# Kernel tuning notes

Hardware: AMD Instinct MI355X
Metric: run time of the kernel (lower is better)

## Reference

```python
import jax, jax.numpy as jnp
import numpy as np
from jax import lax

EPS = 1e-5

def bn(x, g, b):
    # training-mode BatchNorm2d over (N, H, W)
    m = jnp.mean(x, axis=(0, 2, 3), keepdims=True)
    v = jnp.var(x, axis=(0, 2, 3), keepdims=True)
    return (x - m) * lax.rsqrt(v + EPS) * g[None, :, None, None] + b[None, :, None, None]

def conv1x1(x, W):
    # x: [b,c,h,w], W: [o,c]
    return jnp.einsum('bchw,oc->bohw', x, W)

def conv3x3(x, W):
    # W: [o,i,3,3]
    return lax.conv_general_dilated(x, W, (1, 1), 'SAME',
                                    dimension_numbers=('NCHW', 'OIHW', 'NCHW'))

def lga(x, Wqkv, Wproj, g, b):
    # LinearGlobalAttention: O(N) global attention
    bsz, c, h, w = x.shape
    qkv = conv1x1(x, Wqkv)                       # [b, 3c, h, w]
    q, k, v = jnp.split(qkv, 3, axis=1)
    q = q.reshape(bsz, c, h * w)                 # [b, c, N]
    k = jax.nn.softmax(k.reshape(bsz, c, h * w), axis=-1)
    v = v.reshape(bsz, c, h * w)
    ctx = jnp.einsum('bcn,bdn->bcd', k, v)       # [b, c, c]
    out = jnp.einsum('bcd,bcn->bdn', ctx, q)     # context^T @ q -> [b, c, N]
    out = out.reshape(bsz, c, h, w)
    return jax.nn.relu(bn(conv1x1(out, Wproj), g, b))


def setup_inputs() -> dict:
    key = jax.random.key(0)
    ks = jax.random.split(key, 12)
    B, Cin, Cout, H, W = 16, 128, 256, 64, 64
    wd = Cout // 4  # branch width = 64
    sc = 0.05
    inp = {
        'x': jax.random.normal(ks[0], (B, Cin, H, W), jnp.float32),
        'W_sc': jax.random.normal(ks[1], (Cout, Cin), jnp.float32) * sc,
        'g_sc': jnp.ones((Cout,), jnp.float32),
        'b_sc': jnp.zeros((Cout,), jnp.float32),
        'W1': jax.random.normal(ks[2], (Cout, Cin), jnp.float32) * sc,
        'g1': jnp.ones((Cout,), jnp.float32),
        'b1': jnp.zeros((Cout,), jnp.float32),
        'Wb0': jax.random.normal(ks[3], (wd, wd), jnp.float32) * sc,
        'gb0': jnp.ones((wd,), jnp.float32),
        'bb0': jnp.zeros((wd,), jnp.float32),
        'Wb1': jax.random.normal(ks[4], (wd, wd, 3, 3), jnp.float32) * sc,
        'gb1': jnp.ones((wd,), jnp.float32),
        'bb1': jnp.zeros((wd,), jnp.float32),
        'Wqkv2': jax.random.normal(ks[5], (3 * wd, wd), jnp.float32) * sc,
        'Wproj2': jax.random.normal(ks[6], (wd, wd), jnp.float32) * sc,
        'ga2': jnp.ones((wd,), jnp.float32),
        'ba2': jnp.zeros((wd,), jnp.float32),
        'Wqkv3': jax.random.normal(ks[7], (3 * wd, wd), jnp.float32) * sc,
        'Wproj3': jax.random.normal(ks[8], (wd, wd), jnp.float32) * sc,
        'ga3': jnp.ones((wd,), jnp.float32),
        'ba3': jnp.zeros((wd,), jnp.float32),
        'W2': jax.random.normal(ks[9], (Cout, Cout), jnp.float32) * sc,
        'g2': jnp.ones((Cout,), jnp.float32),
        'b2': jnp.zeros((Cout,), jnp.float32),
    }
    return inp


def reference(x, W_sc, g_sc, b_sc, W1, g1, b1,
              Wb0, gb0, bb0, Wb1, gb1, bb1,
              Wqkv2, Wproj2, ga2, ba2,
              Wqkv3, Wproj3, ga3, ba3,
              W2, g2, b2):
    residual = bn(conv1x1(x, W_sc), g_sc, b_sc)
    h = jax.nn.relu(bn(conv1x1(x, W1), g1, b1))      # [b, 256, H, W]
    s0, s1, s2, s3 = jnp.split(h, 4, axis=1)          # width = 64 each
    o0 = jax.nn.relu(bn(conv1x1(s0, Wb0), gb0, bb0))  # k=1 branch
    o1 = jax.nn.relu(bn(conv3x3(s1, Wb1), gb1, bb1))  # k=3 branch
    o2 = lga(s2, Wqkv2, Wproj2, ga2, ba2)             # k=5 -> attention
    o3 = lga(s3, Wqkv3, Wproj3, ga3, ba3)             # k=7 -> attention
    out = jnp.concatenate([o0, o1, o2, o3], axis=1)
    out = bn(conv1x1(out, W2), g2, b2) + residual
    return jax.nn.relu(out)
```

## Files before the change

kernel.cpp:

```cpp
#include <hip/hip_runtime.h>
#include <hip/hip_bf16.h>

using bf16 = __hip_bfloat16;
typedef __bf16 bf16v8 __attribute__((ext_vector_type(8)));
typedef float f32x4 __attribute__((ext_vector_type(4)));

#define HW 4096
#define ROWS 65536

#define AS1 const __attribute__((address_space(1))) void*
#define AS3 __attribute__((address_space(3))) void*

__global__ void r5_init(float* __restrict__ stats) {
    int i = blockIdx.x * 256 + threadIdx.x;
    stats[i] = 0.f;
}

__global__ void r4_cvt_x(const float* __restrict__ x, bf16* __restrict__ xT) {
    __shared__ bf16 tile[64 * 65];
    int b = blockIdx.z, c0 = blockIdx.y * 64, n0 = blockIdx.x * 64;
    int t = threadIdx.x;
    for (int i = 0; i < 16; i++) {
        int idx = i * 256 + t;
        int cc = idx >> 6, nn = idx & 63;
        tile[nn * 65 + cc] = __float2bfloat16(x[((size_t)(b * 128 + c0 + cc)) * HW + n0 + nn]);
    }
    __syncthreads();
    for (int i = 0; i < 16; i++) {
        int idx = i * 256 + t;
        int nn = idx >> 6, cc = idx & 63;
        xT[((size_t)(b * HW + n0 + nn)) * 128 + c0 + cc] = tile[nn * 65 + cc];
    }
}

__global__ void r4_cvt_w(const float* __restrict__ Wsc, const float* __restrict__ W1,
                         const float* __restrict__ Wb0,
                         const float* __restrict__ Wqkv2, const float* __restrict__ Wqkv3,
                         const float* __restrict__ W2, bf16* __restrict__ wbase) {
    int i = blockIdx.x * 256 + threadIdx.x;
    const float* s; int off;
    if      (i < 32768)  { s = Wsc;   off = i; }
    else if (i < 65536)  { s = W1;    off = i - 32768; }
    else if (i < 69632)  { s = Wb0;   off = i - 65536; }
    else if (i < 81920)  { s = Wqkv2; off = i - 69632; }
    else if (i < 94208)  { s = Wqkv3; off = i - 81920; }
    else                 { s = W2;    off = i - 94208; }
    wbase[i] = __float2bfloat16(s[off]);
}

__global__ void r4_pack3(const float* __restrict__ w, bf16* __restrict__ wp) {
    int i = blockIdx.x * 256 + threadIdx.x;
    int tap = i / 4096, rem = i % 4096;
    int o = rem >> 6, c = rem & 63;
    wp[i] = __float2bfloat16(w[(size_t)(o * 64 + c) * 9 + tap]);
}

__global__ __launch_bounds__(256) void r10_act(bf16* __restrict__ buf,
        const float* __restrict__ sums,
        const float* __restrict__ g0, const float* __restrict__ b0,
        const float* __restrict__ g1, const float* __restrict__ b1,
        const float* __restrict__ g2, const float* __restrict__ b2,
        const float* __restrict__ g3, const float* __restrict__ b3,
        int quarter) {
    __shared__ float scS[256], shS[256];
    int t = threadIdx.x;
    {
        const float *gp, *bp; int ci;
        if (quarter) {
            int qi = t >> 6; ci = t & 63;
            gp = qi == 0 ? g0 : qi == 1 ? g1 : qi == 2 ? g2 : g3;
            bp = qi == 0 ? b0 : qi == 1 ? b1 : qi == 2 ? b2 : b3;
        } else { gp = g0; bp = b0; ci = t; }
        float mean = sums[t] * (1.f / 65536.f);
        float var  = sums[256 + t] * (1.f / 65536.f) - mean * mean;
        float s = gp[ci] * rsqrtf(var + 1e-5f);
        scS[t] = s;
        shS[t] = bp[ci] - mean * s;
    }
    __syncthreads();
    long base = (long)blockIdx.x * 8192;
    int c0 = (t & 31) * 8;
#pragma unroll
    for (int i = 0; i < 4; i++) {
        long e = base + i * 2048 + t * 8;
        bf16v8 v = *(const bf16v8*)&buf[e];
#pragma unroll
        for (int j = 0; j < 8; j++) {
            float f = (float)v[j] * scS[c0 + j] + shS[c0 + j];
            v[j] = (__bf16)fmaxf(f, 0.f);
        }
        *(bf16v8*)&buf[e] = v;
    }
}

template <int KK>
__global__ __launch_bounds__(256) void ga_gemm(
        const bf16* __restrict__ A, int a_stride,
        const bf16* __restrict__ W, int w_stride,
        bf16* __restrict__ out0, bf16* __restrict__ out1, int split,
        int out_stride,
        float* __restrict__ stat0, float* __restrict__ stat1,
        int scol0, int scol1) {
    __shared__ bf16 shmem[128 * 136];
    __shared__ float sredS[256], sredQ[256];
    bf16* As = shmem;
    bf16* Ws = shmem + 8192;

    int t = threadIdx.x;
    int wave = t >> 6, lane = t & 63;
    int lo = lane & 15, quad = lane >> 4;
    int wr = wave >> 1, wc = wave & 1;
    int b = blockIdx.z;
    long grow = (long)b * HW + blockIdx.x * 128;
    int o0 = blockIdx.y * 128;
    const bf16* Wb = W + (long)o0 * w_stride;

    f32x4 acc[4][4];
#pragma unroll
    for (int m = 0; m < 4; m++)
#pragma unroll
        for (int n = 0; n < 4; n++) acc[m][n] = (f32x4){0.f, 0.f, 0.f, 0.f};

#pragma unroll
    for (int ph = 0; ph < KK / 64; ph++) {
        int k0 = ph * 64;
#pragma unroll
        for (int j = 0; j < 4; j++) {
            int i = j * 4 + wave;
            int ci = i * 64 + lane;
            int R = ci >> 3, cc = ci & 7;
            int sw = ((cc ^ (R & 7)) << 3);
            __builtin_amdgcn_global_load_lds(
                (AS1)(A + (grow + R) * (long)a_stride + k0 + sw),
                (AS3)(As + i * 512), 16, 0, 0);
            __builtin_amdgcn_global_load_lds(
                (AS1)(Wb + (long)R * w_stride + k0 + sw),
                (AS3)(Ws + i * 512), 16, 0, 0);
        }
        asm volatile("s_waitcnt vmcnt(0)" ::: "memory");
        __syncthreads();
#pragma unroll
        for (int ks = 0; ks < 64; ks += 32) {
            int kk = (ks >> 3) + quad;
            bf16v8 av[4], wv[4];
#pragma unroll
            for (int m = 0; m < 4; m++) {
                int R = wr * 64 + m * 16 + lo;
                av[m] = *(const bf16v8*)&As[R * 64 + ((kk ^ (R & 7)) << 3)];
            }
#pragma unroll
            for (int n = 0; n < 4; n++) {
                int R = wc * 64 + n * 16 + lo;
                wv[n] = *(const bf16v8*)&Ws[R * 64 + ((kk ^ (R & 7)) << 3)];
            }
#pragma unroll
            for (int m = 0; m < 4; m++)
#pragma unroll
                for (int n = 0; n < 4; n++)
                    acc[m][n] = __builtin_amdgcn_mfma_f32_16x16x32_bf16(av[m], wv[n], acc[m][n], 0, 0, 0);
        }
        __syncthreads();
    }

    bf16* Ot = shmem;
#pragma unroll
    for (int m = 0; m < 4; m++)
#pragma unroll
        for (int n = 0; n < 4; n++)
#pragma unroll
            for (int r = 0; r < 4; r++)
                Ot[(wr * 64 + m * 16 + quad * 4 + r) * 136 + wc * 64 + n * 16 + lo] =
                    __float2bfloat16(acc[m][n][r]);
    __syncthreads();
    bool low = o0 < split;
    bf16* op = low ? out0 : out1;
    int oc0 = low ? o0 : o0 - split;
#pragma unroll
    for (int i = 0; i < 8; i++) {
        int u = i * 256 + t;
        int lr = u >> 4, cg = u & 15;
        *(bf16v8*)&op[(grow + lr) * (long)out_stride + oc0 + cg * 8] =
            *(const bf16v8*)&Ot[lr * 136 + cg * 8];
    }
    if (stat0) {
        int c = t & 127, half = t >> 7;
        float s = 0.f, q = 0.f;
#pragma unroll
        for (int r = 0; r < 64; r++) {
            float v = __bfloat162float(Ot[(half * 64 + r) * 136 + c]);
            s += v; q += v * v;
        }
        sredS[t] = s; sredQ[t] = q;
        __syncthreads();
        if (t < 128) {
            float ss = sredS[t] + sredS[t + 128];
            float qq = sredQ[t] + sredQ[t + 128];
            float* st = low ? stat0 : stat1;
            int ci = (low ? scol0 + o0 : scol1 + o0 - split) + c;
            atomicAdd(&st[ci], ss);
            atomicAdd(&st[256 + ci], qq);
        }
    }
}

__global__ __launch_bounds__(256) void gb_gemm(
        const bf16* __restrict__ A, int a_stride,
        const bf16* __restrict__ W, long w_bstride,
        bf16* __restrict__ out, int out_stride,
        float* __restrict__ stat, int scol) {
    __shared__ bf16 shmem[256 * 64 + 64 * 64];
    __shared__ float sredS[256], sredQ[256];
    bf16* As = shmem;
    bf16* Ws = shmem + 256 * 64;

    int t = threadIdx.x;
    int wave = t >> 6, lane = t & 63;
    int lo = lane & 15, quad = lane >> 4;
    int b = blockIdx.z;
    long grow = (long)b * HW + blockIdx.x * 256;
    const bf16* Wb = W + (long)blockIdx.y * 4096 + (long)b * w_bstride;

    f32x4 acc[4][4];
#pragma unroll
    for (int m = 0; m < 4; m++)
#pragma unroll
        for (int n = 0; n < 4; n++) acc[m][n] = (f32x4){0.f, 0.f, 0.f, 0.f};

#pragma unroll
    for (int j = 0; j < 8; j++) {
        int ci = (j * 4 + wave) * 64 + lane;
        int R = ci >> 3, cc = ci & 7;
        __builtin_amdgcn_global_load_lds(
            (AS1)(A + (grow + R) * (long)a_stride + ((cc ^ (R & 7)) << 3)),
            (AS3)(As + (j * 4 + wave) * 512), 16, 0, 0);
    }
#pragma unroll
    for (int j = 0; j < 2; j++) {
        int ci = (j * 4 + wave) * 64 + lane;
        int R = ci >> 3, cc = ci & 7;
        __builtin_amdgcn_global_load_lds(
            (AS1)(Wb + R * 64 + ((cc ^ (R & 7)) << 3)),
            (AS3)(Ws + (j * 4 + wave) * 512), 16, 0, 0);
    }
    asm volatile("s_waitcnt vmcnt(0)" ::: "memory");
    __syncthreads();

#pragma unroll
    for (int ks = 0; ks < 64; ks += 32) {
        bf16v8 av[4], wv[4];
#pragma unroll
        for (int m = 0; m < 4; m++) {
            int R = wave * 64 + m * 16 + lo;
            av[m] = *(const bf16v8*)&As[R * 64 + ((((ks >> 3) + quad) ^ (R & 7)) << 3)];
        }
#pragma unroll
        for (int n = 0; n < 4; n++) {
            int o = n * 16 + lo;
            wv[n] = *(const bf16v8*)&Ws[o * 64 + ((((ks >> 3) + quad) ^ (o & 7)) << 3)];
        }
#pragma unroll
        for (int m = 0; m < 4; m++)
#pragma unroll
            for (int n = 0; n < 4; n++)
                acc[m][n] = __builtin_amdgcn_mfma_f32_16x16x32_bf16(av[m], wv[n], acc[m][n], 0, 0, 0);
    }
    __syncthreads();

    bf16* Ot = shmem;
#pragma unroll
    for (int m = 0; m < 4; m++)
#pragma unroll
        for (int n = 0; n < 4; n++)
#pragma unroll
            for (int r = 0; r < 4; r++)
                Ot[(wave * 64 + m * 16 + quad * 4 + r) * 72 + n * 16 + lo] =
                    __float2bfloat16(acc[m][n][r]);
    __syncthreads();
    int oc0 = blockIdx.y * 64;
#pragma unroll
    for (int i = 0; i < 8; i++) {
        int u = i * 256 + t;
        int lr = u >> 3, cg = u & 7;
        *(bf16v8*)&out[(grow + lr) * (long)out_stride + oc0 + cg * 8] =
            *(const bf16v8*)&Ot[lr * 72 + cg * 8];
    }
    if (stat) {
        int c = t & 63, qtr = t >> 6;
        float s = 0.f, q = 0.f;
#pragma unroll
        for (int r = 0; r < 64; r++) {
            float v = __bfloat162float(Ot[(qtr * 64 + r) * 72 + c]);
            s += v; q += v * v;
        }
        sredS[t] = s; sredQ[t] = q;
        __syncthreads();
        if (t < 64) {
            float ss = sredS[t] + sredS[t + 64] + sredS[t + 128] + sredS[t + 192];
            float qq = sredQ[t] + sredQ[t + 64] + sredQ[t + 128] + sredQ[t + 192];
            atomicAdd(&stat[scol + t], ss);
            atomicAdd(&stat[256 + scol + t], qq);
        }
    }
}

__global__ __launch_bounds__(256) void r12_conv3(
        const bf16* __restrict__ hT, const bf16* __restrict__ wp,
        bf16* __restrict__ obuf, float* __restrict__ stat) {
    __shared__ bf16 As[6 * 66 * 64];
    __shared__ bf16 Wt[9 * 64 * 64];
    __shared__ float sredS[256], sredQ[256];

    int t = threadIdx.x;
    int wave = t >> 6, lane = t & 63;
    int lo = lane & 15, quad = lane >> 4;
    int b = blockIdx.y, y0 = blockIdx.x * 4;

#pragma unroll
    for (int j = 0; j < 18; j++) {
        int i = j * 4 + wave;
        int ci = i * 64 + lane;
        int tap = ci >> 9, rem = ci & 511, o = rem >> 3, ck = rem & 7;
        __builtin_amdgcn_global_load_lds(
            (AS1)(wp + tap * 4096 + o * 64 + ((ck ^ (o & 7)) << 3)),
            (AS3)(Wt + i * 512), 16, 0, 0);
    }
#pragma unroll
    for (int j = 0; j < 12; j++) {
        int i = j * 4 + wave;
        int row = i >> 3, seg = i & 7;
        int yy = y0 - 1 + row;
        if (yy >= 0 && yy < 64) {
            int xg = seg * 8 + (lane >> 3), ck = lane & 7;
            __builtin_amdgcn_global_load_lds(
                (AS1)(hT + ((long)b * HW + yy * 64 + xg) * 256 + 64 + ((ck ^ (xg & 7)) << 3)),
                (AS3)(As + row * 4224 + 64 + seg * 512), 16, 0, 0);
        } else {
            *(bf16v8*)&As[row * 4224 + 64 + seg * 512 + lane * 8] = (bf16v8){0,0,0,0,0,0,0,0};
        }
    }
    if (t < 96) {
        int yr = t >> 4, side = (t >> 3) & 1, ck = t & 7;
        *(bf16v8*)&As[yr * 4224 + (side ? 65 : 0) * 64 + ck * 8] = (bf16v8){0,0,0,0,0,0,0,0};
    }
    asm volatile("s_waitcnt vmcnt(0)" ::: "memory");
    __syncthreads();

    f32x4 acc[4][4];
#pragma unroll
    for (int m = 0; m < 4; m++)
#pragma unroll
        for (int n = 0; n < 4; n++) acc[m][n] = (f32x4){0.f, 0.f, 0.f, 0.f};

#pragma unroll
    for (int tap = 0; tap < 9; tap++) {
        int dy = tap / 3 - 1, dx = tap % 3 - 1;
        int yr = wave + 1 + dy;
#pragma unroll
        for (int ks8 = 0; ks8 < 8; ks8 += 4) {
            int kk = ks8 + quad;
            bf16v8 wv[4];
#pragma unroll
            for (int ot = 0; ot < 4; ot++) {
                int o = ot * 16 + lo;
                wv[ot] = *(const bf16v8*)&Wt[tap * 4096 + o * 64 + ((kk ^ (o & 7)) << 3)];
            }
#pragma unroll
            for (int m = 0; m < 4; m++) {
                int xp = m * 16 + lo + dx;
                bf16v8 av = *(const bf16v8*)&As[yr * 4224 + (xp + 1) * 64 + ((kk ^ (xp & 7)) << 3)];
#pragma unroll
                for (int ot = 0; ot < 4; ot++)
                    acc[m][ot] = __builtin_amdgcn_mfma_f32_16x16x32_bf16(av, wv[ot], acc[m][ot], 0, 0, 0);
            }
        }
    }
    __syncthreads();

    bf16* Ot = As;
#pragma unroll
    for (int m = 0; m < 4; m++)
#pragma unroll
        for (int ot = 0; ot < 4; ot++)
#pragma unroll
            for (int r = 0; r < 4; r++)
                Ot[(wave * 64 + m * 16 + quad * 4 + r) * 72 + ot * 16 + lo] =
                    __float2bfloat16(acc[m][ot][r]);
    __syncthreads();

    long grow = (long)b * HW + y0 * 64;
#pragma unroll
    for (int i = 0; i < 8; i++) {
        int u = i * 256 + t;
        int lr = u >> 3, cg = u & 7;
        *(bf16v8*)&obuf[(grow + lr) * 256 + 64 + cg * 8] = *(const bf16v8*)&Ot[lr * 72 + cg * 8];
    }
    {
        int c = t & 63, qtr = t >> 6;
        float s = 0.f, q = 0.f;
#pragma unroll
        for (int r = 0; r < 64; r++) {
            float v = __bfloat162float(Ot[(qtr * 64 + r) * 72 + c]);
            s += v; q += v * v;
        }
        sredS[t] = s; sredQ[t] = q;
        __syncthreads();
        if (t < 64) {
            float ss = sredS[t] + sredS[t + 64] + sredS[t + 128] + sredS[t + 192];
            float qq = sredQ[t] + sredQ[t + 64] + sredQ[t + 128] + sredQ[t + 192];
            atomicAdd(&stat[64 + t], ss);
            atomicAdd(&stat[256 + 64 + t], qq);
        }
    }
}

__global__ __launch_bounds__(256) void r14_softctx(
        const bf16* __restrict__ qkvT,
        float* __restrict__ ctx_p, float* __restrict__ lpart) {
    __shared__ bf16 Ks[64 * 136];
    __shared__ bf16 Vs[64 * 136];
    __shared__ float red[32 * 64];
    int t = threadIdx.x;
    int wave = t >> 6, lane = t & 63;
    int lo = lane & 15, quad = lane >> 4;
    int b = blockIdx.y, bx = blockIdx.x;

    f32x4 acc[4];
#pragma unroll
    for (int ot = 0; ot < 4; ot++) acc[ot] = (f32x4){0.f, 0.f, 0.f, 0.f};
    float sm[8];
#pragma unroll
    for (int j = 0; j < 8; j++) sm[j] = 0.f;

    for (int it = 0; it < 2; it++) {
        long n0 = ((long)bx * 2 + it) * 128;
        __syncthreads();
#pragma unroll
        for (int sub = 0; sub < 4; sub++) {
            int r = sub * 32 + (t >> 3), cg = t & 7;
            const bf16* row = qkvT + ((long)b * HW + n0 + r) * 192;
            bf16v8 k8 = *(const bf16v8*)(row + 64 + cg * 8);
            bf16v8 v8 = *(const bf16v8*)(row + 128 + cg * 8);
#pragma unroll
            for (int j = 0; j < 8; j++) {
                int c = cg * 8 + j;
                float e = expf((float)k8[j]);
                sm[j] += e;
                Ks[c * 136 + r] = __float2bfloat16(e);
                Vs[c * 136 + r] = (bf16)v8[j];
            }
        }
        __syncthreads();
#pragma unroll
        for (int ks = 0; ks < 128; ks += 32) {
            bf16v8 av = *(const bf16v8*)&Ks[(wave * 16 + lo) * 136 + ks + quad * 8];
#pragma unroll
            for (int ot = 0; ot < 4; ot++) {
                bf16v8 bv = *(const bf16v8*)&Vs[(ot * 16 + lo) * 136 + ks + quad * 8];
                acc[ot] = __builtin_amdgcn_mfma_f32_16x16x32_bf16(av, bv, acc[ot], 0, 0, 0);
            }
        }
    }
    long blk = (long)b * 16 + bx;
#pragma unroll
    for (int ot = 0; ot < 4; ot++) {
#pragma unroll
        for (int r = 0; r < 4; r++) {
            int c = wave * 16 + quad * 4 + r;
            int d = ot * 16 + lo;
            ctx_p[(blk * 64 + c) * 64 + d] = acc[ot][r];
        }
    }
    {
        int rg = t >> 3, cg = t & 7;
#pragma unroll
        for (int j = 0; j < 8; j++) red[rg * 64 + cg * 8 + j] = sm[j];
        __syncthreads();
        if (t < 64) {
            float s = 0.f;
#pragma unroll
            for (int i = 0; i < 32; i++) s += red[i * 64 + t];
            lpart[blk * 64 + t] = s;
        }
    }
}

__global__ __launch_bounds__(256) void r15_mproj(
        const float* __restrict__ Wp, const float* __restrict__ ctx_p,
        const float* __restrict__ lpart, bf16* __restrict__ M) {
    __shared__ float ctxS[16 * 68];
    __shared__ float ilS[16];
    int b = blockIdx.x, qq = blockIdx.y, t = threadIdx.x;
    int e = t & 63, cg = t >> 6;
#pragma unroll
    for (int i = 0; i < 4; i++) {
        int u = i * 256 + t;
        int c_l = u >> 6, d = u & 63;
        float s = 0.f;
#pragma unroll
        for (int p = 0; p < 16; p++)
            s += ctx_p[(((long)b * 16 + p) * 64 + qq * 16 + c_l) * 64 + d];
        ctxS[c_l * 68 + d] = s;
    }
    if (t < 16) {
        float l = 0.f;
#pragma unroll
        for (int p = 0; p < 16; p++)
            l += lpart[((long)b * 16 + p) * 64 + qq * 16 + t];
        ilS[t] = 1.f / l;
    }
    float wreg[64];
#pragma unroll
    for (int i = 0; i < 16; i++) {
        float4 v = *(const float4*)&Wp[e * 64 + i * 4];
        wreg[i * 4 + 0] = v.x; wreg[i * 4 + 1] = v.y;
        wreg[i * 4 + 2] = v.z; wreg[i * 4 + 3] = v.w;
    }
    __syncthreads();
#pragma unroll
    for (int ci = 0; ci < 4; ci++) {
        int c_l = cg * 4 + ci;
        float a = 0.f;
#pragma unroll
        for (int dg = 0; dg < 16; dg++) {
            float4 cv = *(const float4*)&ctxS[c_l * 68 + dg * 4];
            a += wreg[dg * 4 + 0] * cv.x + wreg[dg * 4 + 1] * cv.y
               + wreg[dg * 4 + 2] * cv.z + wreg[dg * 4 + 3] * cv.w;
        }
        M[(long)b * 4096 + e * 64 + qq * 16 + c_l] = __float2bfloat16(a * ilS[c_l]);
    }
}

__global__ void r6_final(const bf16* __restrict__ y2, const bf16* __restrict__ ysc,
                         const float* __restrict__ s2sums, const float* __restrict__ scsums,
                         const float* __restrict__ g2, const float* __restrict__ b2,
                         const float* __restrict__ gsc, const float* __restrict__ bsc,
                         float* __restrict__ out) {
    __shared__ float lo_[64 * 65];
    __shared__ float sc2[64], sh2[64], scc[64], shc[64];
    int b = blockIdx.z, c0 = blockIdx.y * 64, n0 = blockIdx.x * 64;
    int t = threadIdx.x;
    if (t < 64) {
        int ch = c0 + t;
        float m2 = s2sums[ch] * (1.f / 65536.f);
        float v2 = s2sums[256 + ch] * (1.f / 65536.f) - m2 * m2;
        float s = g2[ch] * rsqrtf(v2 + 1e-5f);
        sc2[t] = s; sh2[t] = b2[ch] - m2 * s;
        float mc = scsums[ch] * (1.f / 65536.f);
        float vc = scsums[256 + ch] * (1.f / 65536.f) - mc * mc;
        float s2_ = gsc[ch] * rsqrtf(vc + 1e-5f);
        scc[t] = s2_; shc[t] = bsc[ch] - mc * s2_;
    }
    __syncthreads();
    for (int half = 0; half < 2; half++) {
        int r = half * 32 + (t >> 3), cc = (t & 7) * 8;
        long row = (long)b * HW + n0 + r;
        bf16v8 a8 = *(const bf16v8*)&y2[row * 256 + c0 + cc];
        bf16v8 s8 = *(const bf16v8*)&ysc[row * 256 + c0 + cc];
#pragma unroll
        for (int j = 0; j < 8; j++) {
            int c = cc + j;
            float v = (float)a8[j] * sc2[c] + sh2[c] + (float)s8[j] * scc[c] + shc[c];
            lo_[c * 65 + r] = fmaxf(v, 0.f);
        }
    }
    __syncthreads();
    for (int i = 0; i < 16; i++) {
        int idx = i * 256 + t; int c = idx >> 6, r = idx & 63;
        out[((long)b * 256 + c0 + c) * HW + n0 + r] = lo_[c * 65 + r];
    }
}

extern "C" void kernel_launch(void* const* d_in, const int* in_sizes, int n_in,
                              void* d_out, int out_size, void* d_ws, size_t ws_size,
                              hipStream_t stream) {
    const float* x     = (const float*)d_in[0];
    const float* Wsc   = (const float*)d_in[1];
    const float* gsc   = (const float*)d_in[2];
    const float* bsc   = (const float*)d_in[3];
    const float* W1    = (const float*)d_in[4];
    const float* g1    = (const float*)d_in[5];
    const float* b1    = (const float*)d_in[6];
    const float* Wb0   = (const float*)d_in[7];
    const float* gb0   = (const float*)d_in[8];
    const float* bb0   = (const float*)d_in[9];
    const float* Wb1   = (const float*)d_in[10];
    const float* gb1   = (const float*)d_in[11];
    const float* bb1   = (const float*)d_in[12];
    const float* Wqkv2 = (const float*)d_in[13];
    const float* Wproj2= (const float*)d_in[14];
    const float* ga2   = (const float*)d_in[15];
    const float* ba2   = (const float*)d_in[16];
    const float* Wqkv3 = (const float*)d_in[17];
    const float* Wproj3= (const float*)d_in[18];
    const float* ga3   = (const float*)d_in[19];
    const float* ba3   = (const float*)d_in[20];
    const float* W2    = (const float*)d_in[21];
    const float* g2    = (const float*)d_in[22];
    const float* b2    = (const float*)d_in[23];

    char* ws = (char*)d_ws;
    float* stats = (float*)ws;
    bf16*  M     = (bf16*)(ws + 32768);
    bf16*  wbase = (bf16*)(ws + 163840);
    bf16*  wsc_b = wbase;
    bf16*  wb0_b = wbase + 65536;
    bf16*  wq2_b = wbase + 69632;
    bf16*  wq3_b = wbase + 81920;
    bf16*  w2_b  = wbase + 94208;
    bf16*  wb1p  = (bf16*)(ws + 483328);
    bf16*  xT    = (bf16*)(ws + 1048576);
    float* ctx_p = (float*)(ws + 1048576);
    float* lpart = (float*)(ws + 1048576 + 4194304);
    bf16*  ysc   = (bf16*)(ws + 17825792);
    bf16*  y1    = (bf16*)(ws + 51380224);
    bf16*  y2    = y1;
    bf16*  obuf  = (bf16*)d_out;
    bf16*  qkv   = (bf16*)((char*)d_out + 33554432);

    r5_init<<<dim3(8), 256, 0, stream>>>(stats);
    r4_cvt_w<<<dim3(624), 256, 0, stream>>>(Wsc, W1, Wb0, Wqkv2, Wqkv3, W2, wbase);
    r4_pack3<<<dim3(144), 256, 0, stream>>>(Wb1, wb1p);
    r4_cvt_x<<<dim3(64, 2, 16), 256, 0, stream>>>(x, xT);

    ga_gemm<128><<<dim3(32, 4, 16), 256, 0, stream>>>(
        xT, 128, wsc_b, 128,
        ysc, y1, 256, 256, stats, stats + 512, 0, 0);
    r10_act<<<dim3(2048), 256, 0, stream>>>(y1, stats + 512,
        g1, b1, g1, b1, g1, b1, g1, b1, 0);

    gb_gemm<<<dim3(16, 1, 16), 256, 0, stream>>>(
        y1, 256, wb0_b, 0, obuf, 256, stats + 1024, 0);
    r12_conv3<<<dim3(16, 16), 256, 0, stream>>>(y1, wb1p, obuf, stats + 1024);

    gb_gemm<<<dim3(16, 3, 16), 256, 0, stream>>>(
        y1 + 128, 256, wq2_b, 0, qkv, 192, nullptr, 0);
    r14_softctx<<<dim3(16, 16), 256, 0, stream>>>(qkv, ctx_p, lpart);
    r15_mproj<<<dim3(16, 4), 256, 0, stream>>>(Wproj2, ctx_p, lpart, M);
    gb_gemm<<<dim3(16, 1, 16), 256, 0, stream>>>(
        qkv, 192, M, 4096, obuf + 128, 256, stats + 1024, 128);

    gb_gemm<<<dim3(16, 3, 16), 256, 0, stream>>>(
        y1 + 192, 256, wq3_b, 0, qkv, 192, nullptr, 0);
    r14_softctx<<<dim3(16, 16), 256, 0, stream>>>(qkv, ctx_p, lpart);
    r15_mproj<<<dim3(16, 4), 256, 0, stream>>>(Wproj3, ctx_p, lpart, M);
    gb_gemm<<<dim3(16, 1, 16), 256, 0, stream>>>(
        qkv, 192, M, 4096, obuf + 192, 256, stats + 1024, 192);

    r10_act<<<dim3(2048), 256, 0, stream>>>(obuf, stats + 1024,
        gb0, bb0, gb1, bb1, ga2, ba2, ga3, ba3, 1);
    ga_gemm<256><<<dim3(32, 2, 16), 256, 0, stream>>>(
        obuf, 256, w2_b, 256,
        y2, y2, 1 << 28, 256, stats + 1536, stats + 1536, 0, 0);

    r6_final<<<dim3(64, 4, 16), 256, 0, stream>>>(y2, ysc, stats + 1536, stats + 0,
                                                  g2, b2, gsc, bsc, (float*)d_out);
}
```

Baseline: 329.3 us.

## Batch both attention branches and the k=1 conv into merged launches

Merges the k=1 branch conv and both attention branches' QKV projections into one grid launch, and batches softmax-context, M projection and output GEMM across the two attention branches using an extra grid dimension. Q, K and V are now written to separate contiguous buffers instead of one interleaved 192-wide array. Stats zeroing is folded into the weight conversion kernel. The aim is fewer small kernel launches and larger grids that fill the GPU better. The cost is a reshuffled workspace layout and wider per-launch branching.

```diff
diff --git a/kernel.cpp b/kernel.cpp
--- a/kernel.cpp
+++ b/kernel.cpp
@@ -7,13 +7,26 @@
 
 #define HW 4096
 #define ROWS 65536
+#define BRSTRIDE 4194304
 
 #define AS1 const __attribute__((address_space(1))) void*
 #define AS3 __attribute__((address_space(3))) void*
 
-__global__ void r5_init(float* __restrict__ stats) {
+__global__ void r4_cvt_w(const float* __restrict__ Wsc, const float* __restrict__ W1,
+                         const float* __restrict__ Wb0,
+                         const float* __restrict__ Wqkv2, const float* __restrict__ Wqkv3,
+                         const float* __restrict__ W2, bf16* __restrict__ wbase,
+                         float* __restrict__ stats) {
     int i = blockIdx.x * 256 + threadIdx.x;
-    stats[i] = 0.f;
+    if (i < 2048) stats[i] = 0.f;
+    const float* s; int off;
+    if      (i < 32768)  { s = Wsc;   off = i; }
+    else if (i < 65536)  { s = W1;    off = i - 32768; }
+    else if (i < 69632)  { s = Wb0;   off = i - 65536; }
+    else if (i < 81920)  { s = Wqkv2; off = i - 69632; }
+    else if (i < 94208)  { s = Wqkv3; off = i - 81920; }
+    else                 { s = W2;    off = i - 94208; }
+    wbase[i] = __float2bfloat16(s[off]);
 }
 
 __global__ void r4_cvt_x(const float* __restrict__ x, bf16* __restrict__ xT) {
@@ -31,21 +44,6 @@
         int nn = idx >> 6, cc = idx & 63;
         xT[((size_t)(b * HW + n0 + nn)) * 128 + c0 + cc] = tile[nn * 65 + cc];
     }
-}
-
-__global__ void r4_cvt_w(const float* __restrict__ Wsc, const float* __restrict__ W1,
-                         const float* __restrict__ Wb0,
-                         const float* __restrict__ Wqkv2, const float* __restrict__ Wqkv3,
-                         const float* __restrict__ W2, bf16* __restrict__ wbase) {
-    int i = blockIdx.x * 256 + threadIdx.x;
-    const float* s; int off;
-    if      (i < 32768)  { s = Wsc;   off = i; }
-    else if (i < 65536)  { s = W1;    off = i - 32768; }
-    else if (i < 69632)  { s = Wb0;   off = i - 65536; }
-    else if (i < 81920)  { s = Wqkv2; off = i - 69632; }
-    else if (i < 94208)  { s = Wqkv3; off = i - 81920; }
-    else                 { s = W2;    off = i - 94208; }
-    wbase[i] = __float2bfloat16(s[off]);
 }
 
 __global__ void r4_pack3(const float* __restrict__ w, bf16* __restrict__ wp) {
@@ -203,11 +201,12 @@
     }
 }
 
-__global__ __launch_bounds__(256) void gb_gemm(
-        const bf16* __restrict__ A, int a_stride,
-        const bf16* __restrict__ W, long w_bstride,
-        bf16* __restrict__ out, int out_stride,
-        float* __restrict__ stat, int scol) {
+__global__ __launch_bounds__(256) void gq_gemm(
+        const bf16* __restrict__ y1,
+        const bf16* __restrict__ wq2, const bf16* __restrict__ wq3,
+        const bf16* __restrict__ wb0,
+        bf16* __restrict__ qs, bf16* __restrict__ ks, bf16* __restrict__ vs,
+        bf16* __restrict__ obuf, float* __restrict__ stats) {
     __shared__ bf16 shmem[256 * 64 + 64 * 64];
     __shared__ float sredS[256], sredQ[256];
     bf16* As = shmem;
@@ -216,9 +215,19 @@
     int t = threadIdx.x;
     int wave = t >> 6, lane = t & 63;
     int lo = lane & 15, quad = lane >> 4;
-    int b = blockIdx.z;
+    int b = blockIdx.z, y = blockIdx.y;
     long grow = (long)b * HW + blockIdx.x * 256;
-    const bf16* Wb = W + (long)blockIdx.y * 4096 + (long)b * w_bstride;
+
+    const bf16* Ab; const bf16* Wb; bf16* outp; int ostride; float* st;
+    if (y == 6) {
+        Ab = y1; Wb = wb0; outp = obuf; ostride = 256; st = stats;
+    } else {
+        int br = y / 3, sel = y - br * 3;
+        Ab = y1 + 128 + br * 64;
+        Wb = (br ? wq3 : wq2) + sel * 4096;
+        outp = (sel == 0 ? qs : sel == 1 ? ks : vs) + (long)br * BRSTRIDE;
+        ostride = 64; st = nullptr;
+    }
 
     f32x4 acc[4][4];
 #pragma unroll
@@ -231,7 +240,7 @@
         int ci = (j * 4 + wave) * 64 + lane;
         int R = ci >> 3, cc = ci & 7;
         __builtin_amdgcn_global_load_lds(
-            (AS1)(A + (grow + R) * (long)a_stride + ((cc ^ (R & 7)) << 3)),
+            (AS1)(Ab + (grow + R) * 256L + ((cc ^ (R & 7)) << 3)),
             (AS3)(As + (j * 4 + wave) * 512), 16, 0, 0);
     }
 #pragma unroll
@@ -246,17 +255,17 @@
     __syncthreads();
 
 #pragma unroll
-    for (int ks = 0; ks < 64; ks += 32) {
+    for (int ks_ = 0; ks_ < 64; ks_ += 32) {
         bf16v8 av[4], wv[4];
 #pragma unroll
         for (int m = 0; m < 4; m++) {
             int R = wave * 64 + m * 16 + lo;
-            av[m] = *(const bf16v8*)&As[R * 64 + ((((ks >> 3) + quad) ^ (R & 7)) << 3)];
+            av[m] = *(const bf16v8*)&As[R * 64 + ((((ks_ >> 3) + quad) ^ (R & 7)) << 3)];
         }
 #pragma unroll
         for (int n = 0; n < 4; n++) {
             int o = n * 16 + lo;
-            wv[n] = *(const bf16v8*)&Ws[o * 64 + ((((ks >> 3) + quad) ^ (o & 7)) << 3)];
+            wv[n] = *(const bf16v8*)&Ws[o * 64 + ((((ks_ >> 3) + quad) ^ (o & 7)) << 3)];
         }
 #pragma unroll
         for (int m = 0; m < 4; m++)
@@ -276,15 +285,14 @@
                 Ot[(wave * 64 + m * 16 + quad * 4 + r) * 72 + n * 16 + lo] =
                     __float2bfloat16(acc[m][n][r]);
     __syncthreads();
-    int oc0 = blockIdx.y * 64;
 #pragma unroll
     for (int i = 0; i < 8; i++) {
         int u = i * 256 + t;
         int lr = u >> 3, cg = u & 7;
-        *(bf16v8*)&out[(grow + lr) * (long)out_stride + oc0 + cg * 8] =
+        *(bf16v8*)&outp[(grow + lr) * (long)ostride + cg * 8] =
             *(const bf16v8*)&Ot[lr * 72 + cg * 8];
     }
-    if (stat) {
+    if (st) {
         int c = t & 63, qtr = t >> 6;
         float s = 0.f, q = 0.f;
 #pragma unroll
@@ -297,8 +305,107 @@
         if (t < 64) {
             float ss = sredS[t] + sredS[t + 64] + sredS[t + 128] + sredS[t + 192];
             float qq = sredQ[t] + sredQ[t + 64] + sredQ[t + 128] + sredQ[t + 192];
-            atomicAdd(&stat[scol + t], ss);
-            atomicAdd(&stat[256 + scol + t], qq);
+            atomicAdd(&st[t], ss);
+            atomicAdd(&st[256 + t], qq);
+        }
+    }
+}
+
+__global__ __launch_bounds__(256) void gp_gemm(
+        const bf16* __restrict__ qs, const bf16* __restrict__ M,
+        bf16* __restrict__ obuf, float* __restrict__ stats) {
+    __shared__ bf16 shmem[256 * 64 + 64 * 64];
+    __shared__ float sredS[256], sredQ[256];
+    bf16* As = shmem;
+    bf16* Ws = shmem + 256 * 64;
+
+    int t = threadIdx.x;
+    int wave = t >> 6, lane = t & 63;
+    int lo = lane & 15, quad = lane >> 4;
+    int b = blockIdx.z, y = blockIdx.y;
+    long grow = (long)b * HW + blockIdx.x * 256;
+    const bf16* Ab = qs + (long)y * BRSTRIDE;
+    const bf16* Wb = M + y * 65536 + (long)b * 4096;
+    int oc0 = 128 + y * 64;
+
+    f32x4 acc[4][4];
+#pragma unroll
+    for (int m = 0; m < 4; m++)
+#pragma unroll
+        for (int n = 0; n < 4; n++) acc[m][n] = (f32x4){0.f, 0.f, 0.f, 0.f};
+
+#pragma unroll
+    for (int j = 0; j < 8; j++) {
+        int ci = (j * 4 + wave) * 64 + lane;
+        int R = ci >> 3, cc = ci & 7;
+        __builtin_amdgcn_global_load_lds(
+            (AS1)(Ab + (grow + R) * 64L + ((cc ^ (R & 7)) << 3)),
+            (AS3)(As + (j * 4 + wave) * 512), 16, 0, 0);
+    }
+#pragma unroll
+    for (int j = 0; j < 2; j++) {
+        int ci = (j * 4 + wave) * 64 + lane;
+        int R = ci >> 3, cc = ci & 7;
+        __builtin_amdgcn_global_load_lds(
+            (AS1)(Wb + R * 64 + ((cc ^ (R & 7)) << 3)),
+            (AS3)(Ws + (j * 4 + wave) * 512), 16, 0, 0);
+    }
+    asm volatile("s_waitcnt vmcnt(0)" ::: "memory");
+    __syncthreads();
+
+#pragma unroll
+    for (int ks_ = 0; ks_ < 64; ks_ += 32) {
+        bf16v8 av[4], wv[4];
+#pragma unroll
+        for (int m = 0; m < 4; m++) {
+            int R = wave * 64 + m * 16 + lo;
+            av[m] = *(const bf16v8*)&As[R * 64 + ((((ks_ >> 3) + quad) ^ (R & 7)) << 3)];
+        }
+#pragma unroll
+        for (int n = 0; n < 4; n++) {
+            int o = n * 16 + lo;
+            wv[n] = *(const bf16v8*)&Ws[o * 64 + ((((ks_ >> 3) + quad) ^ (o & 7)) << 3)];
+        }
+#pragma unroll
+        for (int m = 0; m < 4; m++)
+#pragma unroll
+            for (int n = 0; n < 4; n++)
+                acc[m][n] = __builtin_amdgcn_mfma_f32_16x16x32_bf16(av[m], wv[n], acc[m][n], 0, 0, 0);
+    }
+    __syncthreads();
+
+    bf16* Ot = shmem;
+#pragma unroll
+    for (int m = 0; m < 4; m++)
+#pragma unroll
+        for (int n = 0; n < 4; n++)
+#pragma unroll
+            for (int r = 0; r < 4; r++)
+                Ot[(wave * 64 + m * 16 + quad * 4 + r) * 72 + n * 16 + lo] =
+                    __float2bfloat16(acc[m][n][r]);
+    __syncthreads();
+#pragma unroll
+    for (int i = 0; i < 8; i++) {
+        int u = i * 256 + t;
+        int lr = u >> 3, cg = u & 7;
+        *(bf16v8*)&obuf[(grow + lr) * 256L + oc0 + cg * 8] =
+            *(const bf16v8*)&Ot[lr * 72 + cg * 8];
+    }
+    {
+        int c = t & 63, qtr = t >> 6;
+        float s = 0.f, q = 0.f;
+#pragma unroll
+        for (int r = 0; r < 64; r++) {
+            float v = __bfloat162float(Ot[(qtr * 64 + r) * 72 + c]);
+            s += v; q += v * v;
+        }
+        sredS[t] = s; sredQ[t] = q;
+        __syncthreads();
+        if (t < 64) {
+            float ss = sredS[t] + sredS[t + 64] + sredS[t + 128] + sredS[t + 192];
+            float qq = sredQ[t] + sredQ[t + 64] + sredQ[t + 128] + sredQ[t + 192];
+            atomicAdd(&stats[oc0 + t], ss);
+            atomicAdd(&stats[256 + oc0 + t], qq);
         }
     }
 }
@@ -414,7 +521,7 @@
 }
 
 __global__ __launch_bounds__(256) void r14_softctx(
-        const bf16* __restrict__ qkvT,
+        const bf16* __restrict__ ks_t, const bf16* __restrict__ vs_t,
         float* __restrict__ ctx_p, float* __restrict__ lpart) {
     __shared__ bf16 Ks[64 * 136];
     __shared__ bf16 Vs[64 * 136];
@@ -422,7 +529,9 @@
     int t = threadIdx.x;
     int wave = t >> 6, lane = t & 63;
     int lo = lane & 15, quad = lane >> 4;
-    int b = blockIdx.y, bx = blockIdx.x;
+    int b = blockIdx.y, bx = blockIdx.x, z = blockIdx.z;
+    const bf16* kb = ks_t + (long)z * BRSTRIDE;
+    const bf16* vb = vs_t + (long)z * BRSTRIDE;
 
     f32x4 acc[4];
 #pragma unroll
@@ -437,9 +546,9 @@
 #pragma unroll
         for (int sub = 0; sub < 4; sub++) {
             int r = sub * 32 + (t >> 3), cg = t & 7;
-            const bf16* row = qkvT + ((long)b * HW + n0 + r) * 192;
-            bf16v8 k8 = *(const bf16v8*)(row + 64 + cg * 8);
-            bf16v8 v8 = *(const bf16v8*)(row + 128 + cg * 8);
+            long row = (long)b * HW + n0 + r;
+            bf16v8 k8 = *(const bf16v8*)(kb + row * 64 + cg * 8);
+            bf16v8 v8 = *(const bf16v8*)(vb + row * 64 + cg * 8);
 #pragma unroll
             for (int j = 0; j < 8; j++) {
                 int c = cg * 8 + j;
@@ -460,7 +569,7 @@
             }
         }
     }
-    long blk = (long)b * 16 + bx;
+    long blk = ((long)z * 16 + b) * 16 + bx;
 #pragma unroll
     for (int ot = 0; ot < 4; ot++) {
 #pragma unroll
@@ -485,12 +594,15 @@
 }
 
 __global__ __launch_bounds__(256) void r15_mproj(
-        const float* __restrict__ Wp, const float* __restrict__ ctx_p,
-        const float* __restrict__ lpart, bf16* __restrict__ M) {
+        const float* __restrict__ Wp2, const float* __restrict__ Wp3,
+        const float* __restrict__ ctx_p, const float* __restrict__ lpart,
+        bf16* __restrict__ M) {
     __shared__ float ctxS[16 * 68];
     __shared__ float ilS[16];
-    int b = blockIdx.x, qq = blockIdx.y, t = threadIdx.x;
+    int b = blockIdx.x, qq = blockIdx.y, z = blockIdx.z, t = threadIdx.x;
     int e = t & 63, cg = t >> 6;
+    const float* Wp = z ? Wp3 : Wp2;
+    long zb = (long)z * 16 + b;
 #pragma unroll
     for (int i = 0; i < 4; i++) {
         int u = i * 256 + t;
@@ -498,14 +610,14 @@
         float s = 0.f;
 #pragma unroll
         for (int p = 0; p < 16; p++)
-            s += ctx_p[(((long)b * 16 + p) * 64 + qq * 16 + c_l) * 64 + d];
+            s += ctx_p[((zb * 16 + p) * 64 + qq * 16 + c_l) * 64 + d];
         ctxS[c_l * 68 + d] = s;
     }
     if (t < 16) {
         float l = 0.f;
 #pragma unroll
         for (int p = 0; p < 16; p++)
-            l += lpart[((long)b * 16 + p) * 64 + qq * 16 + t];
+            l += lpart[(zb * 16 + p) * 64 + qq * 16 + t];
         ilS[t] = 1.f / l;
     }
     float wreg[64];
@@ -526,7 +638,8 @@
             a += wreg[dg * 4 + 0] * cv.x + wreg[dg * 4 + 1] * cv.y
                + wreg[dg * 4 + 2] * cv.z + wreg[dg * 4 + 3] * cv.w;
         }
-        M[(long)b * 4096 + e * 64 + qq * 16 + c_l] = __float2bfloat16(a * ilS[c_l]);
+        M[(long)z * 65536 + (long)b * 4096 + e * 64 + qq * 16 + c_l] =
+            __float2bfloat16(a * ilS[c_l]);
     }
 }
 
@@ -601,24 +714,25 @@
     char* ws = (char*)d_ws;
     float* stats = (float*)ws;
     bf16*  M     = (bf16*)(ws + 32768);
-    bf16*  wbase = (bf16*)(ws + 163840);
+    bf16*  wbase = (bf16*)(ws + 294912);
     bf16*  wsc_b = wbase;
     bf16*  wb0_b = wbase + 65536;
     bf16*  wq2_b = wbase + 69632;
     bf16*  wq3_b = wbase + 81920;
     bf16*  w2_b  = wbase + 94208;
-    bf16*  wb1p  = (bf16*)(ws + 483328);
+    bf16*  wb1p  = (bf16*)(ws + 614400);
     bf16*  xT    = (bf16*)(ws + 1048576);
-    float* ctx_p = (float*)(ws + 1048576);
-    float* lpart = (float*)(ws + 1048576 + 4194304);
+    bf16*  vs    = (bf16*)(ws + 1048576);
     bf16*  ysc   = (bf16*)(ws + 17825792);
     bf16*  y1    = (bf16*)(ws + 51380224);
+    float* ctx_p = (float*)(ws + 51380224);
+    float* lpart = (float*)(ws + 51380224 + 8388608);
     bf16*  y2    = y1;
     bf16*  obuf  = (bf16*)d_out;
-    bf16*  qkv   = (bf16*)((char*)d_out + 33554432);
-
-    r5_init<<<dim3(8), 256, 0, stream>>>(stats);
-    r4_cvt_w<<<dim3(624), 256, 0, stream>>>(Wsc, W1, Wb0, Wqkv2, Wqkv3, W2, wbase);
+    bf16*  qs    = (bf16*)((char*)d_out + 33554432);
+    bf16*  ks    = (bf16*)((char*)d_out + 50331648);
+
+    r4_cvt_w<<<dim3(624), 256, 0, stream>>>(Wsc, W1, Wb0, Wqkv2, Wqkv3, W2, wbase, stats);
     r4_pack3<<<dim3(144), 256, 0, stream>>>(Wb1, wb1p);
     r4_cvt_x<<<dim3(64, 2, 16), 256, 0, stream>>>(x, xT);
 
@@ -628,23 +742,13 @@
     r10_act<<<dim3(2048), 256, 0, stream>>>(y1, stats + 512,
         g1, b1, g1, b1, g1, b1, g1, b1, 0);
 
-    gb_gemm<<<dim3(16, 1, 16), 256, 0, stream>>>(
-        y1, 256, wb0_b, 0, obuf, 256, stats + 1024, 0);
     r12_conv3<<<dim3(16, 16), 256, 0, stream>>>(y1, wb1p, obuf, stats + 1024);
-
-    gb_gemm<<<dim3(16, 3, 16), 256, 0, stream>>>(
-        y1 + 128, 256, wq2_b, 0, qkv, 192, nullptr, 0);
-    r14_softctx<<<dim3(16, 16), 256, 0, stream>>>(qkv, ctx_p, lpart);
-    r15_mproj<<<dim3(16, 4), 256, 0, stream>>>(Wproj2, ctx_p, lpart, M);
-    gb_gemm<<<dim3(16, 1, 16), 256, 0, stream>>>(
-        qkv, 192, M, 4096, obuf + 128, 256, stats + 1024, 128);
-
-    gb_gemm<<<dim3(16, 3, 16), 256, 0, stream>>>(
-        y1 + 192, 256, wq3_b, 0, qkv, 192, nullptr, 0);
-    r14_softctx<<<dim3(16, 16), 256, 0, stream>>>(qkv, ctx_p, lpart);
-    r15_mproj<<<dim3(16, 4), 256, 0, stream>>>(Wproj3, ctx_p, lpart, M);
-    gb_gemm<<<dim3(16, 1, 16), 256, 0, stream>>>(
-        qkv, 192, M, 4096, obuf + 192, 256, stats + 1024, 192);
+    gq_gemm<<<dim3(16, 7, 16), 256, 0, stream>>>(
+        y1, wq2_b, wq3_b, wb0_b, qs, ks, vs, obuf, stats + 1024);
+
+    r14_softctx<<<dim3(16, 16, 2), 256, 0, stream>>>(ks, vs, ctx_p, lpart);
+    r15_mproj<<<dim3(16, 4, 2), 256, 0, stream>>>(Wproj2, Wproj3, ctx_p, lpart, M);
+    gp_gemm<<<dim3(16, 2, 16), 256, 0, stream>>>(qs, M, obuf, stats + 1024);
 
     r10_act<<<dim3(2048), 256, 0, stream>>>(obuf, stats + 1024,
         gb0, bb0, gb1, bb1, ga2, ba2, ga3, ba3, 1);
```

Result: faster. 291.3 us (-11.5%).
